# Optimization experiments

Hardware: AMD Instinct MI355X
Metric: run time of the kernel (lower is better)

## Reference

```python
import jax, jax.numpy as jnp
import numpy as np

N_EMBD = 1024
N_HEAD = 16
HEAD_DIM = N_EMBD // N_HEAD


def setup_inputs() -> dict:
    key = jax.random.key(0)
    kx, kq, kk, kv, ko = jax.random.split(key, 5)
    B, T, C = 2, 2048, N_EMBD
    s = 1.0 / np.sqrt(C)
    return {
        "x": jax.random.normal(kx, (B, T, C), dtype=jnp.float32),
        "Wq": jax.random.normal(kq, (C, C), dtype=jnp.float32) * s,
        "Wk": jax.random.normal(kk, (C, C), dtype=jnp.float32) * s,
        "Wv": jax.random.normal(kv, (C, C), dtype=jnp.float32) * s,
        "Wo": jax.random.normal(ko, (C, C), dtype=jnp.float32) * s,
    }


def reference(x, Wq, Wk, Wv, Wo):
    B, T, C = x.shape
    H, D = N_HEAD, HEAD_DIM
    # projections (torch Linear: y = x @ W^T)
    q = (x @ Wq.T).reshape(B, T, H, D).transpose(0, 2, 1, 3)  # [B,H,T,D]
    k = (x @ Wk.T).reshape(B, T, H, D).transpose(0, 2, 1, 3)
    v = (x @ Wv.T).reshape(B, T, H, D).transpose(0, 2, 1, 3)
    scale = 1.0 / np.sqrt(D).astype(np.float32)
    scores = jnp.einsum("bhqd,bhkd->bhqk", q, k) * scale  # [B,H,T,T]
    causal = jnp.tril(jnp.ones((T, T), dtype=bool))
    scores = jnp.where(causal, scores, -jnp.inf)
    attn = jax.nn.softmax(scores, axis=-1)
    y = jnp.einsum("bhqk,bhkd->bhqd", attn, v)  # [B,H,T,D]
    y = y.transpose(0, 2, 1, 3).reshape(B, T, C)
    return y @ Wo.T
```

## Files before the change

kernel.cpp:

```cpp
#include <hip/hip_runtime.h>
#include <hip/hip_bf16.h>
#include <math.h>

#define SEQ   2048
#define CDIM  1024
#define NH    16
#define HD    64

#define K_SCALE 0.1803368801111204f

typedef __attribute__((ext_vector_type(8))) short bf16x8;
typedef __attribute__((ext_vector_type(4))) float f32x4;
typedef __attribute__((ext_vector_type(4))) short short4v;

__device__ __forceinline__ short f2bf(float f) {
  return (short)__builtin_bit_cast(unsigned short, __float2bfloat16(f));
}

__device__ __forceinline__ void glds16(const short* g, short* l) {
  __builtin_amdgcn_global_load_lds(
      (const __attribute__((address_space(1))) unsigned int*)g,
      (__attribute__((address_space(3))) unsigned int*)l, 16, 0, 0);
}

__global__ void cvt_kernel(const float* __restrict__ src, short* __restrict__ dst, int n4) {
  int i = blockIdx.x * blockDim.x + threadIdx.x;
  if (i >= n4) return;
  float4 v = reinterpret_cast<const float4*>(src)[i];
  short4v o;
  o.x = f2bf(v.x); o.y = f2bf(v.y); o.z = f2bf(v.z); o.w = f2bf(v.w);
  reinterpret_cast<short4v*>(dst)[i] = o;
}

__global__ void cvtw_kernel(const float* __restrict__ w0, const float* __restrict__ w1,
                            const float* __restrict__ w2, const float* __restrict__ w3,
                            short* __restrict__ d0, short* __restrict__ d1,
                            short* __restrict__ d2, short* __restrict__ d3) {
  const int y = blockIdx.y;
  const float* src = (y == 0) ? w0 : (y == 1) ? w1 : (y == 2) ? w2 : w3;
  short* dst       = (y == 0) ? d0 : (y == 1) ? d1 : (y == 2) ? d2 : d3;
  const float mult = (y == 1) ? K_SCALE : 1.0f;
  int i = blockIdx.x * blockDim.x + threadIdx.x;
  float4 v = reinterpret_cast<const float4*>(src)[i];
  short4v o;
  o.x = f2bf(v.x * mult); o.y = f2bf(v.y * mult);
  o.z = f2bf(v.z * mult); o.w = f2bf(v.w * mult);
  reinterpret_cast<short4v*>(dst)[i] = o;
}

template<int MODE, int BN>
__global__ __launch_bounds__(256)
void gemm_bt(const short* __restrict__ A,
             const short* __restrict__ W0, const short* __restrict__ W1, const short* __restrict__ W2,
             short* __restrict__ ob0, short* __restrict__ ob1, short* __restrict__ ob2,
             float* __restrict__ of)
{
  constexpr int K = CDIM;
  constexpr int NJF = BN / 32;
  const int z = (MODE == 0) ? blockIdx.z : 0;
  const short* W;
  short* outb = nullptr;
  if (MODE == 0) {
    W    = (z == 0) ? W0  : (z == 1) ? W1  : W2;
    outb = (z == 0) ? ob0 : (z == 1) ? ob1 : ob2;
  } else {
    W = W0;
  }
  const int m0 = blockIdx.y * 128;
  const int n0 = blockIdx.x * BN;

  __shared__ __align__(16) short As[128 * 32];
  __shared__ __align__(16) short Bs[BN * 32];

  const int tid  = threadIdx.x;
  const int lane = tid & 63;
  const int wid  = tid >> 6;
  const int wr   = wid >> 1;
  const int wc   = wid & 1;
  const int rl   = lane & 15;
  const int g    = lane >> 4;

  f32x4 acc[4][NJF];
#pragma unroll
  for (int i = 0; i < 4; ++i)
#pragma unroll
    for (int j = 0; j < NJF; ++j)
      acc[i][j] = (f32x4){0.f, 0.f, 0.f, 0.f};

  const int lrow = lane >> 2;
  const int lcol = (lane & 3) * 8;
  const int arow = wid * 32 + lrow;

  for (int kt = 0; kt < K / 32; ++kt) {
    const int k0 = kt * 32;
    glds16(&A[(size_t)(m0 + arow) * K + k0 + lcol],      &As[(wid * 32) * 32]);
    glds16(&A[(size_t)(m0 + arow + 16) * K + k0 + lcol], &As[(wid * 32 + 16) * 32]);
    if constexpr (BN == 128) {
      glds16(&W[(size_t)(n0 + arow) * K + k0 + lcol],      &Bs[(wid * 32) * 32]);
      glds16(&W[(size_t)(n0 + arow + 16) * K + k0 + lcol], &Bs[(wid * 32 + 16) * 32]);
    } else {
      glds16(&W[(size_t)(n0 + wid * 16 + lrow) * K + k0 + lcol], &Bs[(wid * 16) * 32]);
    }
    __syncthreads();

    bf16x8 af[4], bfr[NJF];
#pragma unroll
    for (int mi = 0; mi < 4; ++mi)
      af[mi] = *(const bf16x8*)&As[(wr * 64 + mi * 16 + rl) * 32 + g * 8];
#pragma unroll
    for (int nj = 0; nj < NJF; ++nj)
      bfr[nj] = *(const bf16x8*)&Bs[(wc * (BN / 2) + nj * 16 + rl) * 32 + g * 8];
#pragma unroll
    for (int mi = 0; mi < 4; ++mi)
#pragma unroll
      for (int nj = 0; nj < NJF; ++nj)
        acc[mi][nj] = __builtin_amdgcn_mfma_f32_16x16x32_bf16(af[mi], bfr[nj], acc[mi][nj], 0, 0, 0);
    __syncthreads();
  }

#pragma unroll
  for (int mi = 0; mi < 4; ++mi) {
#pragma unroll
    for (int nj = 0; nj < NJF; ++nj) {
      const int gmb = m0 + wr * 64 + mi * 16 + g * 4;
      const int gn  = n0 + wc * (BN / 2) + nj * 16 + rl;
      if (MODE == 0 && z == 2) {
        short4v pk;
#pragma unroll
        for (int r = 0; r < 4; ++r) pk[r] = f2bf(acc[mi][nj][r]);
        const int b = gmb >> 11, t = gmb & 2047;
        const int h = gn >> 6,  d = gn & 63;
        *(short4v*)&outb[(((size_t)(b * NH + h)) * HD + d) * SEQ + t] = pk;
      } else {
#pragma unroll
        for (int r = 0; r < 4; ++r) {
          const int gm = gmb + r;
          const float val = acc[mi][nj][r];
          if (MODE == 0) {
            const int b = gm >> 11, t = gm & 2047;
            const int h = gn >> 6,  d = gn & 63;
            outb[(((size_t)(b * NH + h)) * SEQ + t) * HD + d] = f2bf(val);
          } else {
            of[(size_t)gm * CDIM + gn] = val;
          }
        }
      }
    }
  }
}

__global__ __launch_bounds__(256)
void attn_kernel(const short* __restrict__ q, const short* __restrict__ k,
                 const short* __restrict__ vt, short* __restrict__ yb)
{
  const int bh  = blockIdx.y;
  const int pp  = blockIdx.x;
  const int jA  = pp;
  const int jB  = 31 - pp;
  const int tid = threadIdx.x;
  const int lane = tid & 63;
  const int wid  = tid >> 6;
  const int rl   = lane & 15;
  const int g    = lane >> 4;

  const short* Qp = q  + (size_t)bh * SEQ * HD;
  const short* Kp = k  + (size_t)bh * SEQ * HD;
  const short* Vp = vt + (size_t)bh * HD * SEQ;

  __shared__ short Ks[64 * 72];
  __shared__ short Vs[64 * 72];
  __shared__ short Ps[4][2][16 * 72];

  const int q0A = jA * 64 + wid * 16;
  const int q0B = jB * 64 + wid * 16;

  bf16x8 qfA[2], qfB[2];
#pragma unroll
  for (int ds = 0; ds < 2; ++ds) {
    qfA[ds] = *(const bf16x8*)&Qp[(size_t)(q0A + rl) * HD + ds * 32 + g * 8];
    qfB[ds] = *(const bf16x8*)&Qp[(size_t)(q0B + rl) * HD + ds * 32 + g * 8];
  }

  f32x4 accA[4], accB[4];
  float mA[4], lA[4], mB[4], lB[4];
#pragma unroll
  for (int r = 0; r < 4; ++r) { mA[r] = -INFINITY; lA[r] = 0.f; mB[r] = -INFINITY; lB[r] = 0.f; }
#pragma unroll
  for (int nt = 0; nt < 4; ++nt) { accA[nt] = (f32x4){0,0,0,0}; accB[nt] = (f32x4){0,0,0,0}; }

  const int srow = tid >> 3;
  const int scol = (tid & 7) * 8;

  auto process = [&](bf16x8 (&qf)[2], f32x4 (&acc)[4], float (&m_run)[4], float (&l_run)[4],
                     bool diag, int t, int q0w, short* PsW) {
    f32x4 s_[4];
#pragma unroll
    for (int ct = 0; ct < 4; ++ct) s_[ct] = (f32x4){0, 0, 0, 0};
    __builtin_amdgcn_s_setprio(1);
#pragma unroll
    for (int ct = 0; ct < 4; ++ct)
#pragma unroll
      for (int ds = 0; ds < 2; ++ds) {
        bf16x8 kf = *(const bf16x8*)&Ks[(ct * 16 + rl) * 72 + ds * 32 + g * 8];
        s_[ct] = __builtin_amdgcn_mfma_f32_16x16x32_bf16(qf[ds], kf, s_[ct], 0, 0, 0);
      }
    __builtin_amdgcn_s_setprio(0);

    float pm[4] = {-INFINITY, -INFINITY, -INFINITY, -INFINITY};
#pragma unroll
    for (int ct = 0; ct < 4; ++ct)
#pragma unroll
      for (int r = 0; r < 4; ++r) {
        float sv = s_[ct][r];
        if (diag) {
          const int key = t * 64 + ct * 16 + rl;
          const int qq  = q0w + g * 4 + r;
          sv = (key <= qq) ? sv : -INFINITY;
        }
        s_[ct][r] = sv;
        pm[r] = fmaxf(pm[r], sv);
      }

    bool need = false;
#pragma unroll
    for (int r = 0; r < 4; ++r) need = need || (pm[r] > m_run[r]);
    if (__any((int)need)) {
#pragma unroll
      for (int r = 0; r < 4; ++r) {
        pm[r] = fmaxf(pm[r], __shfl_xor(pm[r], 1));
        pm[r] = fmaxf(pm[r], __shfl_xor(pm[r], 2));
        pm[r] = fmaxf(pm[r], __shfl_xor(pm[r], 4));
        pm[r] = fmaxf(pm[r], __shfl_xor(pm[r], 8));
        const float mnew = fmaxf(m_run[r], pm[r]);
        const float f = exp2f(m_run[r] - mnew);
        m_run[r] = mnew;
        l_run[r] *= f;
#pragma unroll
        for (int nt = 0; nt < 4; ++nt) acc[nt][r] *= f;
      }
    }

#pragma unroll
    for (int ct = 0; ct < 4; ++ct) {
      const int c = ct * 16 + rl;
#pragma unroll
      for (int r = 0; r < 4; ++r) {
        const float p = exp2f(s_[ct][r] - m_run[r]);
        l_run[r] += p;
        PsW[(g * 4 + r) * 72 + c] = f2bf(p);
      }
    }

    __builtin_amdgcn_s_setprio(1);
#pragma unroll
    for (int ks = 0; ks < 2; ++ks) {
      bf16x8 pf = *(const bf16x8*)&PsW[rl * 72 + ks * 32 + g * 8];
#pragma unroll
      for (int nt = 0; nt < 4; ++nt) {
        bf16x8 vf = *(const bf16x8*)&Vs[(nt * 16 + rl) * 72 + ks * 32 + g * 8];
        acc[nt] = __builtin_amdgcn_mfma_f32_16x16x32_bf16(pf, vf, acc[nt], 0, 0, 0);
      }
    }
    __builtin_amdgcn_s_setprio(0);
  };

  auto epilogue = [&](f32x4 (&acc)[4], float (&l_run)[4], int q0w) {
    const int b = bh >> 4, h = bh & 15;
#pragma unroll
    for (int r = 0; r < 4; ++r) {
      float lr = l_run[r];
      lr += __shfl_xor(lr, 1);
      lr += __shfl_xor(lr, 2);
      lr += __shfl_xor(lr, 4);
      lr += __shfl_xor(lr, 8);
      const float inv = 1.0f / lr;
      const int qq = q0w + g * 4 + r;
#pragma unroll
      for (int nt = 0; nt < 4; ++nt)
        yb[((size_t)b * SEQ + qq) * CDIM + h * HD + nt * 16 + rl] = f2bf(acc[nt][r] * inv);
    }
  };

  bf16x8 k0 = *(const bf16x8*)&Kp[(size_t)srow * HD + scol];
  bf16x8 k1 = *(const bf16x8*)&Kp[(size_t)(srow + 32) * HD + scol];
  bf16x8 v0 = *(const bf16x8*)&Vp[(size_t)srow * SEQ + scol];
  bf16x8 v1 = *(const bf16x8*)&Vp[(size_t)(srow + 32) * SEQ + scol];

  for (int t = 0; t <= jB; ++t) {
    __syncthreads();
    *(bf16x8*)&Ks[srow * 72 + scol]        = k0;
    *(bf16x8*)&Ks[(srow + 32) * 72 + scol] = k1;
    *(bf16x8*)&Vs[srow * 72 + scol]        = v0;
    *(bf16x8*)&Vs[(srow + 32) * 72 + scol] = v1;
    __syncthreads();

    if (t < jB) {
      const int kn = (t + 1) * 64;
      k0 = *(const bf16x8*)&Kp[(size_t)(kn + srow) * HD + scol];
      k1 = *(const bf16x8*)&Kp[(size_t)(kn + srow + 32) * HD + scol];
      v0 = *(const bf16x8*)&Vp[(size_t)srow * SEQ + kn + scol];
      v1 = *(const bf16x8*)&Vp[(size_t)(srow + 32) * SEQ + kn + scol];
    }

    process(qfB, accB, mB, lB, t == jB, t, q0B, &Ps[wid][0][0]);
    if (t <= jA)
      process(qfA, accA, mA, lA, t == jA, t, q0A, &Ps[wid][1][0]);
  }

  epilogue(accB, lB, q0B);
  epilogue(accA, lA, q0A);
}

extern "C" void kernel_launch(void* const* d_in, const int* in_sizes, int n_in,
                              void* d_out, int out_size, void* d_ws, size_t ws_size,
                              hipStream_t stream) {
  const float* x  = (const float*)d_in[0];
  const float* Wq = (const float*)d_in[1];
  const float* Wk = (const float*)d_in[2];
  const float* Wv = (const float*)d_in[3];
  const float* Wo = (const float*)d_in[4];
  float* out = (float*)d_out;

  char* ws = (char*)d_ws;
  short* xb  = (short*)(ws);
  short* Wqb = (short*)(ws + ((size_t)8  << 20));
  short* Wkb = (short*)(ws + ((size_t)10 << 20));
  short* Wvb = (short*)(ws + ((size_t)12 << 20));
  short* Wob = (short*)(ws + ((size_t)14 << 20));
  short* qb  = (short*)(ws + ((size_t)16 << 20));
  short* kbp = (short*)(ws + ((size_t)24 << 20));
  short* vtp = (short*)(ws + ((size_t)32 << 20));
  short* yb  = (short*)(ws + ((size_t)40 << 20));

  cvt_kernel<<<4096, 256, 0, stream>>>(x, xb, 1048576);
  cvtw_kernel<<<dim3(1024, 4), 256, 0, stream>>>(Wq, Wk, Wv, Wo, Wqb, Wkb, Wvb, Wob);

  gemm_bt<0, 128><<<dim3(8, 32, 3), 256, 0, stream>>>(xb, Wqb, Wkb, Wvb, qb, kbp, vtp, nullptr);

  attn_kernel<<<dim3(16, 32), 256, 0, stream>>>(qb, kbp, vtp, yb);

  gemm_bt<1, 64><<<dim3(16, 32, 1), 256, 0, stream>>>(yb, Wob, nullptr, nullptr,
                                                      nullptr, nullptr, nullptr, out);
}
```

Measured before the change: 135.5 us.

## Widen GEMM K-tile to 64 and double-buffer attention K/V with padded P

The projection GEMM now stages 64-wide K slices per iteration instead of 32, halving the number of barrier pairs and loop trips at the cost of doubled LDS tiles. The attention kernel double-buffers its K/V shared tiles, which removes one __syncthreads per key tile. The per-wave P scratch stride changes from 72 to 68 to alter bank mapping, with P reads split into two 8-byte loads. The single remaining barrier with two buffers relies on the buffer parity to avoid overwrite races, and the extra LDS may reduce occupancy.

```diff
diff --git a/kernel.cpp b/kernel.cpp
--- a/kernel.cpp
+++ b/kernel.cpp
@@ -69,8 +69,8 @@
   const int m0 = blockIdx.y * 128;
   const int n0 = blockIdx.x * BN;
 
-  __shared__ __align__(16) short As[128 * 32];
-  __shared__ __align__(16) short Bs[BN * 32];
+  __shared__ __align__(16) short As[128 * 64];
+  __shared__ __align__(16) short Bs[BN * 64];
 
   const int tid  = threadIdx.x;
   const int lane = tid & 63;
@@ -87,34 +87,42 @@
     for (int j = 0; j < NJF; ++j)
       acc[i][j] = (f32x4){0.f, 0.f, 0.f, 0.f};
 
-  const int lrow = lane >> 2;
-  const int lcol = (lane & 3) * 8;
+  const int lrow = lane >> 3;
+  const int lcol = (lane & 7) * 8;
   const int arow = wid * 32 + lrow;
 
-  for (int kt = 0; kt < K / 32; ++kt) {
-    const int k0 = kt * 32;
-    glds16(&A[(size_t)(m0 + arow) * K + k0 + lcol],      &As[(wid * 32) * 32]);
-    glds16(&A[(size_t)(m0 + arow + 16) * K + k0 + lcol], &As[(wid * 32 + 16) * 32]);
+  for (int kt = 0; kt < K / 64; ++kt) {
+    const int k0 = kt * 64;
+    glds16(&A[(size_t)(m0 + arow) * K + k0 + lcol],      &As[(wid * 32) * 64]);
+    glds16(&A[(size_t)(m0 + arow + 8) * K + k0 + lcol],  &As[(wid * 32 + 8) * 64]);
+    glds16(&A[(size_t)(m0 + arow + 16) * K + k0 + lcol], &As[(wid * 32 + 16) * 64]);
+    glds16(&A[(size_t)(m0 + arow + 24) * K + k0 + lcol], &As[(wid * 32 + 24) * 64]);
     if constexpr (BN == 128) {
-      glds16(&W[(size_t)(n0 + arow) * K + k0 + lcol],      &Bs[(wid * 32) * 32]);
-      glds16(&W[(size_t)(n0 + arow + 16) * K + k0 + lcol], &Bs[(wid * 32 + 16) * 32]);
+      glds16(&W[(size_t)(n0 + arow) * K + k0 + lcol],      &Bs[(wid * 32) * 64]);
+      glds16(&W[(size_t)(n0 + arow + 8) * K + k0 + lcol],  &Bs[(wid * 32 + 8) * 64]);
+      glds16(&W[(size_t)(n0 + arow + 16) * K + k0 + lcol], &Bs[(wid * 32 + 16) * 64]);
+      glds16(&W[(size_t)(n0 + arow + 24) * K + k0 + lcol], &Bs[(wid * 32 + 24) * 64]);
     } else {
-      glds16(&W[(size_t)(n0 + wid * 16 + lrow) * K + k0 + lcol], &Bs[(wid * 16) * 32]);
+      glds16(&W[(size_t)(n0 + wid * 16 + lrow) * K + k0 + lcol],     &Bs[(wid * 16) * 64]);
+      glds16(&W[(size_t)(n0 + wid * 16 + 8 + lrow) * K + k0 + lcol], &Bs[(wid * 16 + 8) * 64]);
     }
     __syncthreads();
 
-    bf16x8 af[4], bfr[NJF];
-#pragma unroll
-    for (int mi = 0; mi < 4; ++mi)
-      af[mi] = *(const bf16x8*)&As[(wr * 64 + mi * 16 + rl) * 32 + g * 8];
-#pragma unroll
-    for (int nj = 0; nj < NJF; ++nj)
-      bfr[nj] = *(const bf16x8*)&Bs[(wc * (BN / 2) + nj * 16 + rl) * 32 + g * 8];
-#pragma unroll
-    for (int mi = 0; mi < 4; ++mi)
+#pragma unroll
+    for (int d2 = 0; d2 < 2; ++d2) {
+      bf16x8 af[4], bfr[NJF];
+#pragma unroll
+      for (int mi = 0; mi < 4; ++mi)
+        af[mi] = *(const bf16x8*)&As[(wr * 64 + mi * 16 + rl) * 64 + d2 * 32 + g * 8];
 #pragma unroll
       for (int nj = 0; nj < NJF; ++nj)
-        acc[mi][nj] = __builtin_amdgcn_mfma_f32_16x16x32_bf16(af[mi], bfr[nj], acc[mi][nj], 0, 0, 0);
+        bfr[nj] = *(const bf16x8*)&Bs[(wc * (BN / 2) + nj * 16 + rl) * 64 + d2 * 32 + g * 8];
+#pragma unroll
+      for (int mi = 0; mi < 4; ++mi)
+#pragma unroll
+        for (int nj = 0; nj < NJF; ++nj)
+          acc[mi][nj] = __builtin_amdgcn_mfma_f32_16x16x32_bf16(af[mi], bfr[nj], acc[mi][nj], 0, 0, 0);
+    }
     __syncthreads();
   }
 
@@ -167,9 +175,9 @@
   const short* Kp = k  + (size_t)bh * SEQ * HD;
   const short* Vp = vt + (size_t)bh * HD * SEQ;
 
-  __shared__ short Ks[64 * 72];
-  __shared__ short Vs[64 * 72];
-  __shared__ short Ps[4][2][16 * 72];
+  __shared__ short Ks[2][64 * 72];
+  __shared__ short Vs[2][64 * 72];
+  __shared__ short Ps[4][2][16 * 68];
 
   const int q0A = jA * 64 + wid * 16;
   const int q0B = jB * 64 + wid * 16;
@@ -192,7 +200,7 @@
   const int scol = (tid & 7) * 8;
 
   auto process = [&](bf16x8 (&qf)[2], f32x4 (&acc)[4], float (&m_run)[4], float (&l_run)[4],
-                     bool diag, int t, int q0w, short* PsW) {
+                     bool diag, int t, int q0w, short* PsW, const short* KsB, const short* VsB) {
     f32x4 s_[4];
 #pragma unroll
     for (int ct = 0; ct < 4; ++ct) s_[ct] = (f32x4){0, 0, 0, 0};
@@ -201,7 +209,7 @@
     for (int ct = 0; ct < 4; ++ct)
 #pragma unroll
       for (int ds = 0; ds < 2; ++ds) {
-        bf16x8 kf = *(const bf16x8*)&Ks[(ct * 16 + rl) * 72 + ds * 32 + g * 8];
+        bf16x8 kf = *(const bf16x8*)&KsB[(ct * 16 + rl) * 72 + ds * 32 + g * 8];
         s_[ct] = __builtin_amdgcn_mfma_f32_16x16x32_bf16(qf[ds], kf, s_[ct], 0, 0, 0);
       }
     __builtin_amdgcn_s_setprio(0);
@@ -247,17 +255,21 @@
       for (int r = 0; r < 4; ++r) {
         const float p = exp2f(s_[ct][r] - m_run[r]);
         l_run[r] += p;
-        PsW[(g * 4 + r) * 72 + c] = f2bf(p);
+        PsW[(g * 4 + r) * 68 + c] = f2bf(p);
       }
     }
 
     __builtin_amdgcn_s_setprio(1);
 #pragma unroll
     for (int ks = 0; ks < 2; ++ks) {
-      bf16x8 pf = *(const bf16x8*)&PsW[rl * 72 + ks * 32 + g * 8];
+      const short4v plo = *(const short4v*)&PsW[rl * 68 + ks * 32 + g * 8];
+      const short4v phi = *(const short4v*)&PsW[rl * 68 + ks * 32 + g * 8 + 4];
+      bf16x8 pf;
+#pragma unroll
+      for (int j = 0; j < 4; ++j) { pf[j] = plo[j]; pf[j + 4] = phi[j]; }
 #pragma unroll
       for (int nt = 0; nt < 4; ++nt) {
-        bf16x8 vf = *(const bf16x8*)&Vs[(nt * 16 + rl) * 72 + ks * 32 + g * 8];
+        bf16x8 vf = *(const bf16x8*)&VsB[(nt * 16 + rl) * 72 + ks * 32 + g * 8];
         acc[nt] = __builtin_amdgcn_mfma_f32_16x16x32_bf16(pf, vf, acc[nt], 0, 0, 0);
       }
     }
@@ -287,11 +299,11 @@
   bf16x8 v1 = *(const bf16x8*)&Vp[(size_t)(srow + 32) * SEQ + scol];
 
   for (int t = 0; t <= jB; ++t) {
-    __syncthreads();
-    *(bf16x8*)&Ks[srow * 72 + scol]        = k0;
-    *(bf16x8*)&Ks[(srow + 32) * 72 + scol] = k1;
-    *(bf16x8*)&Vs[srow * 72 + scol]        = v0;
-    *(bf16x8*)&Vs[(srow + 32) * 72 + scol] = v1;
+    const int cb = t & 1;
+    *(bf16x8*)&Ks[cb][srow * 72 + scol]        = k0;
+    *(bf16x8*)&Ks[cb][(srow + 32) * 72 + scol] = k1;
+    *(bf16x8*)&Vs[cb][srow * 72 + scol]        = v0;
+    *(bf16x8*)&Vs[cb][(srow + 32) * 72 + scol] = v1;
     __syncthreads();
 
     if (t < jB) {
@@ -302,9 +314,9 @@
       v1 = *(const bf16x8*)&Vp[(size_t)(srow + 32) * SEQ + kn + scol];
     }
 
-    process(qfB, accB, mB, lB, t == jB, t, q0B, &Ps[wid][0][0]);
+    process(qfB, accB, mB, lB, t == jB, t, q0B, &Ps[wid][0][0], &Ks[cb][0], &Vs[cb][0]);
     if (t <= jA)
-      process(qfA, accA, mA, lA, t == jA, t, q0A, &Ps[wid][1][0]);
+      process(qfA, accA, mA, lA, t == jA, t, q0A, &Ps[wid][1][0], &Ks[cb][0], &Vs[cb][0]);
   }
 
   epilogue(accB, lB, q0B);
```

New measurement: 158.4 us. 1.17x slower.
